# Performance work log

Measured on AMD Instinct MI355X. Metric: run time of the kernel, lower is better.

Reference implementation:

```python
import jax, jax.numpy as jnp
import numpy as np

L, H, E, D, FF, V, CTX = 8, 16, 1024, 64, 4096, 2048, 2048
B, T = 4, 1024


def _ln(x, g, b, eps=1e-5):
    mu = x.mean(-1, keepdims=True)
    var = ((x - mu) ** 2).mean(-1, keepdims=True)
    return (x - mu) * jax.lax.rsqrt(var + eps) * g + b


def setup_inputs() -> dict:
    key = jax.random.key(0)
    ks = jax.random.split(key, 12)
    s = 0.02
    return {
        "tokens": jax.random.randint(ks[0], (B, T), 0, V),
        "tok_emb": jax.random.normal(ks[1], (V, E), jnp.float32) * s,
        "pos_emb": jax.random.normal(ks[2], (CTX, E), jnp.float32) * s,
        "Wq": jax.random.normal(ks[3], (L, H, E, D), jnp.float32) * s,
        "Wk": jax.random.normal(ks[4], (L, H, E, D), jnp.float32) * s,
        "Wv": jax.random.normal(ks[5], (L, H, E, D), jnp.float32) * s,
        "Wo": jax.random.normal(ks[6], (L, H * D, E), jnp.float32) * s,
        "bo": jnp.zeros((L, E), jnp.float32),
        "ln1_g": jnp.ones((L, E), jnp.float32),
        "ln1_b": jnp.zeros((L, E), jnp.float32),
        "ln2_g": jnp.ones((L, E), jnp.float32),
        "ln2_b": jnp.zeros((L, E), jnp.float32),
        "W1": jax.random.normal(ks[7], (L, E, FF), jnp.float32) * s,
        "b1": jnp.zeros((L, FF), jnp.float32),
        "W2": jax.random.normal(ks[8], (L, FF, E), jnp.float32) * s,
        "b2": jnp.zeros((L, E), jnp.float32),
        "lnf_g": jnp.ones((E,), jnp.float32),
        "lnf_b": jnp.zeros((E,), jnp.float32),
        "Wlm": jax.random.normal(ks[9], (E, V), jnp.float32) * s,
        "blm": jnp.zeros((V,), jnp.float32),
    }


def reference(tokens, tok_emb, pos_emb, Wq, Wk, Wv, Wo, bo, ln1_g, ln1_b,
              ln2_g, ln2_b, W1, b1, W2, b2, lnf_g, lnf_b, Wlm, blm):
    # NOTE: original indexes pos_embd with token ids (pos_embd(x.int()))
    x = tok_emb[tokens] + pos_emb[tokens]  # [B,T,E]
    t = x.shape[1]
    causal = jnp.tril(jnp.ones((t, t), bool))
    scale = 1.0 / jnp.sqrt(jnp.float32(D))
    for l in range(L):
        x = _ln(x, ln1_g[l], ln1_b[l])
        q = jnp.einsum('bte,hed->bhtd', x, Wq[l])
        k = jnp.einsum('bte,hed->bhtd', x, Wk[l])
        v = jnp.einsum('bte,hed->bhtd', x, Wv[l])
        scores = jnp.einsum('bhtd,bhsd->bhts', q, k) * scale
        scores = jnp.where(causal, scores, -jnp.inf)
        att = jax.nn.softmax(scores, axis=-1)
        o = jnp.einsum('bhts,bhsd->bhtd', att, v)
        o = o.transpose(0, 2, 1, 3).reshape(x.shape[0], t, H * D)
        x = x + o @ Wo[l] + bo[l]
        x = _ln(x, ln2_g[l], ln2_b[l])
        x = x + jax.nn.relu(x @ W1[l] + b1[l]) @ W2[l] + b2[l]
    x = _ln(x, lnf_g, lnf_b)
    return x @ Wlm + blm
```

## Files before the change

kernel.cpp:

```cpp
#include <hip/hip_runtime.h>
#include <hip/hip_bf16.h>

#define LAYERS 8
#define H_ 16
#define E_ 1024
#define D_ 64
#define FF_ 4096
#define V_ 2048
#define B_ 4
#define T_ 1024
#define MTOK (B_*T_)

typedef __bf16 bf16x8_t __attribute__((ext_vector_type(8)));
typedef __bf16 bf16x4_t __attribute__((ext_vector_type(4)));
typedef float f32x4_t __attribute__((ext_vector_type(4)));
typedef __hip_bfloat16 bf16_t;

__device__ __forceinline__ bf16_t f2b(float f) { return __float2bfloat16(f); }

__global__ void embed_kernel(const int* __restrict__ tokens,
                             const float* __restrict__ te,
                             const float* __restrict__ pe,
                             bf16_t* __restrict__ x) {
  int row = blockIdx.x;
  int tok = tokens[row];
  int t = threadIdx.x;
  float4 va = ((const float4*)(te + (size_t)tok * E_))[t];
  float4 vp = ((const float4*)(pe + (size_t)tok * E_))[t];
  bf16x4_t o;
  o[0] = (__bf16)(va.x + vp.x); o[1] = (__bf16)(va.y + vp.y);
  o[2] = (__bf16)(va.z + vp.z); o[3] = (__bf16)(va.w + vp.w);
  ((bf16x4_t*)(x + (size_t)row * E_))[t] = o;
}

__global__ __launch_bounds__(256) void ln_kernel(const bf16_t* __restrict__ xin,
                                                 bf16_t* __restrict__ xout,
                                                 const float* __restrict__ g,
                                                 const float* __restrict__ b) {
  int tid = threadIdx.x;
  int row = blockIdx.x * 2 + (tid >> 7);
  int li = tid & 127;
  size_t base = (size_t)row * E_ + li * 8;
  bf16x8_t v8 = *(const bf16x8_t*)(xin + base);
  float z[8];
  float s = 0.f, sq = 0.f;
#pragma unroll
  for (int j = 0; j < 8; j++) { z[j] = (float)v8[j]; s += z[j]; sq += z[j] * z[j]; }
  for (int off = 32; off; off >>= 1) {
    s  += __shfl_xor(s, off, 64);
    sq += __shfl_xor(sq, off, 64);
  }
  __shared__ float2 wred[4];
  if ((tid & 63) == 0) wred[tid >> 6] = make_float2(s, sq);
  __syncthreads();
  int wb = (tid >> 7) << 1;
  float S = wred[wb].x + wred[wb + 1].x, SQ = wred[wb].y + wred[wb + 1].y;
  float mean = S * (1.0f / E_);
  float var  = SQ * (1.0f / E_) - mean * mean;
  float inv = rsqrtf(var + 1e-5f);
  float4 g0 = *(const float4*)(g + li * 8), g1 = *(const float4*)(g + li * 8 + 4);
  float4 b0 = *(const float4*)(b + li * 8), b1 = *(const float4*)(b + li * 8 + 4);
  float gg[8] = {g0.x, g0.y, g0.z, g0.w, g1.x, g1.y, g1.z, g1.w};
  float bb[8] = {b0.x, b0.y, b0.z, b0.w, b1.x, b1.y, b1.z, b1.w};
  bf16x8_t o;
#pragma unroll
  for (int j = 0; j < 8; j++) o[j] = (__bf16)((z[j] - mean) * inv * gg[j] + bb[j]);
  *(bf16x8_t*)(xout + base) = o;
}

__global__ __launch_bounds__(256) void reduce_ln_kernel(
    const bf16_t* __restrict__ p,
    const bf16_t* __restrict__ tin,
    const float* __restrict__ bias,
    bf16_t* __restrict__ r,
    bf16_t* __restrict__ tout,
    const float* __restrict__ g,
    const float* __restrict__ b) {
  int tid = threadIdx.x;
  int row = blockIdx.x * 2 + (tid >> 7);
  int li = tid & 127;
  size_t base = (size_t)row * E_ + li * 8;
  bf16x8_t tv = *(const bf16x8_t*)(tin + base);
  bf16x8_t p0 = *(const bf16x8_t*)(p + base);
  bf16x8_t p1 = *(const bf16x8_t*)(p + (size_t)MTOK * E_ + base);
  float4 c0 = *(const float4*)(bias + li * 8), c1 = *(const float4*)(bias + li * 8 + 4);
  float bb[8] = {c0.x, c0.y, c0.z, c0.w, c1.x, c1.y, c1.z, c1.w};
  bf16x8_t rv;
  float z[8];
  float s = 0.f, sq = 0.f;
#pragma unroll
  for (int j = 0; j < 8; j++) {
    float y = (float)tv[j] + (float)p0[j] + (float)p1[j] + bb[j];
    rv[j] = (__bf16)y;
    z[j] = (float)rv[j];
    s += z[j]; sq += z[j] * z[j];
  }
  *(bf16x8_t*)(r + base) = rv;
  for (int off = 32; off; off >>= 1) {
    s  += __shfl_xor(s, off, 64);
    sq += __shfl_xor(sq, off, 64);
  }
  __shared__ float2 wred[4];
  if ((tid & 63) == 0) wred[tid >> 6] = make_float2(s, sq);
  __syncthreads();
  int wb = (tid >> 7) << 1;
  float S = wred[wb].x + wred[wb + 1].x, SQ = wred[wb].y + wred[wb + 1].y;
  float mean = S * (1.0f / E_);
  float var  = SQ * (1.0f / E_) - mean * mean;
  float inv = rsqrtf(var + 1e-5f);
  float4 g0 = *(const float4*)(g + li * 8), g1 = *(const float4*)(g + li * 8 + 4);
  float4 d0 = *(const float4*)(b + li * 8), d1 = *(const float4*)(b + li * 8 + 4);
  float gg[8] = {g0.x, g0.y, g0.z, g0.w, g1.x, g1.y, g1.z, g1.w};
  float dd[8] = {d0.x, d0.y, d0.z, d0.w, d1.x, d1.y, d1.z, d1.w};
  bf16x8_t o;
#pragma unroll
  for (int j = 0; j < 8; j++) o[j] = (__bf16)((z[j] - mean) * inv * gg[j] + dd[j]);
  *(bf16x8_t*)(tout + base) = o;
}

__global__ __launch_bounds__(256) void prep_weights_kernel(
    const float* __restrict__ Wq, const float* __restrict__ Wk,
    const float* __restrict__ Wv, const float* __restrict__ Wo,
    const float* __restrict__ W1, const float* __restrict__ W2,
    bf16_t* __restrict__ WqkvT, bf16_t* __restrict__ WoT,
    bf16_t* __restrict__ W1T, bf16_t* __restrict__ W2T, int l) {
  __shared__ float tile[64][65];
  int bid = blockIdx.x, tid = threadIdx.x;
  const float* src; bf16_t* dst; int R, C, r0, c0;
  if (bid < 768) {
    int op = bid >> 8, rem = bid & 255;
    int h = rem >> 4, tt = rem & 15;
    const float* W = (op == 0) ? Wq : (op == 1) ? Wk : Wv;
    src = W + (size_t)l * H_ * E_ * D_ + (size_t)h * E_ * D_;
    dst = WqkvT + (size_t)op * E_ * H_ * D_ + (size_t)h * E_ * D_;
    R = E_; C = D_; r0 = tt * 64; c0 = 0;
  } else if (bid < 1024) {
    int tt = bid - 768;
    src = Wo + (size_t)l * H_ * D_ * E_; dst = WoT;
    R = H_ * D_; C = E_; r0 = (tt >> 4) * 64; c0 = (tt & 15) * 64;
  } else if (bid < 2048) {
    int tt = bid - 1024;
    src = W1 + (size_t)l * E_ * FF_; dst = W1T;
    R = E_; C = FF_; r0 = (tt >> 6) * 64; c0 = (tt & 63) * 64;
  } else {
    int tt = bid - 2048;
    src = W2 + (size_t)l * FF_ * E_; dst = W2T;
    R = FF_; C = E_; r0 = (tt >> 4) * 64; c0 = (tt & 15) * 64;
  }
#pragma unroll
  for (int i = 0; i < 4; i++) {
    int idx = i * 256 + tid;
    int row = idx >> 4, q4 = (idx & 15) * 4;
    float4 v = *(const float4*)(src + (size_t)(r0 + row) * C + c0 + q4);
    tile[row][q4 + 0] = v.x; tile[row][q4 + 1] = v.y;
    tile[row][q4 + 2] = v.z; tile[row][q4 + 3] = v.w;
  }
  __syncthreads();
#pragma unroll
  for (int i = 0; i < 2; i++) {
    int idx = i * 256 + tid;
    int c = idx >> 3, r8 = (idx & 7) * 8;
    bf16x8_t ov;
#pragma unroll
    for (int j = 0; j < 8; j++) ov[j] = (__bf16)tile[r8 + j][c];
    *(bf16x8_t*)(dst + (size_t)(c0 + c) * R + r0 + r8) = ov;
  }
}

__global__ void transpose_kernel(const float* __restrict__ in, bf16_t* __restrict__ out,
                                 int R, int C) {
  __shared__ float tile[32][33];
  int r0 = blockIdx.y * 32, c0 = blockIdx.x * 32;
  int tx = threadIdx.x, ty = threadIdx.y;
  for (int i = 0; i < 4; i++)
    tile[ty + i * 8][tx] = in[(size_t)(r0 + ty + i * 8) * C + (c0 + tx)];
  __syncthreads();
  for (int i = 0; i < 4; i++)
    out[(size_t)(c0 + ty + i * 8) * R + (r0 + tx)] = f2b(tile[tx][ty + i * 8]);
}

enum { MODE_F32 = 0, MODE_BF16 = 1, MODE_QKV = 2, MODE_BF16R = 3 };

__device__ __forceinline__ void gload16(const bf16_t* g, bf16_t* l) {
  __builtin_amdgcn_global_load_lds((const __attribute__((address_space(1))) void*)g,
                                   (__attribute__((address_space(3))) void*)l, 16, 0, 0);
}

__device__ __forceinline__ int xcd_swz(int flat, int nwg) {
  int q = nwg >> 3, r = nwg & 7;
  int xcd = flat & 7, idx = flat >> 3;
  return (xcd < r ? xcd * (q + 1) : r * (q + 1) + (xcd - r) * q) + idx;
}

#define BK 32
template <int BM, int BN, int MODE>
__global__ __launch_bounds__(256) void gemm97_kernel(
    const bf16_t* __restrict__ A, long long sAz, int lda,
    const bf16_t* __restrict__ Bt, long long sBz, int ldb,
    void* __restrict__ C, long long sCz,
    const float* __restrict__ bias,
    const void* __restrict__ resid,
    int M, int N, int K, int relu) {
  constexpr int FR = BM / 32, FC = BN / 32;
  constexpr int A_ISS = BM / 64, B_ISS = BN / 64;
  __shared__ __align__(16) bf16_t As[2][BM * BK];
  __shared__ __align__(16) bf16_t Bs[2][BN * BK];
  int tid = threadIdx.x;
  int z = blockIdx.z;
  int nwg = gridDim.x * gridDim.y;
  int flat = xcd_swz(blockIdx.y * gridDim.x + blockIdx.x, nwg);
  int m0 = (flat / gridDim.x) * BM, n0 = (flat % gridDim.x) * BN;
  const bf16_t* Ab = A + (size_t)z * sAz + (size_t)m0 * lda;
  const bf16_t* Bb = Bt + (size_t)z * sBz + (size_t)n0 * ldb;
  int lane = tid & 63, wave = tid >> 6;
  int wr = (wave >> 1) * (BM / 2), wc = (wave & 1) * (BN / 2);
  int lr = lane & 15, lk = (lane >> 4) * 8;
  int srow = tid >> 2;
  int scol = (tid & 3) * 8;

  f32x4_t acc[FR][FC];
  for (int i = 0; i < FR; i++)
    for (int j = 0; j < FC; j++)
      acc[i][j] = (f32x4_t){0.f, 0.f, 0.f, 0.f};

  auto stage = [&](int buf, int k0) {
#pragma unroll
    for (int i = 0; i < A_ISS; i++)
      gload16(Ab + (size_t)(i * 64 + srow) * lda + k0 + scol, &As[buf][i * 2048 + wave * 512]);
#pragma unroll
    for (int i = 0; i < B_ISS; i++)
      gload16(Bb + (size_t)(i * 64 + srow) * ldb + k0 + scol, &Bs[buf][i * 2048 + wave * 512]);
  };

  int nk = K / BK;
  stage(0, 0);
  __syncthreads();
  int cur = 0;
  for (int kt = 0; kt < nk; ++kt) {
    if (kt + 1 < nk) stage(cur ^ 1, (kt + 1) * BK);
    bf16x8_t af[FR], bfv[FC];
#pragma unroll
    for (int i = 0; i < FR; i++)
      af[i] = *(const bf16x8_t*)(&As[cur][(wr + i * 16 + lr) * BK + lk]);
#pragma unroll
    for (int j = 0; j < FC; j++)
      bfv[j] = *(const bf16x8_t*)(&Bs[cur][(wc + j * 16 + lr) * BK + lk]);
#pragma unroll
    for (int i = 0; i < FR; i++)
#pragma unroll
      for (int j = 0; j < FC; j++)
        acc[i][j] = __builtin_amdgcn_mfma_f32_16x16x32_bf16(af[i], bfv[j], acc[i][j], 0, 0, 0);
    __syncthreads();
    cur ^= 1;
  }

#pragma unroll
  for (int i = 0; i < FR; i++)
#pragma unroll
    for (int j = 0; j < FC; j++) {
      f32x4_t v = acc[i][j];
      int n = n0 + wc + j * 16 + lr;
      int mb = m0 + wr + i * 16 + (lane >> 4) * 4;
#pragma unroll
      for (int r = 0; r < 4; r++) {
        int m = mb + r;
        float val = v[r];
        if (bias) val += bias[n];
        if (relu) val = fmaxf(val, 0.f);
        if (MODE == MODE_F32) {
          size_t idx = (size_t)z * sCz + (size_t)m * N + n;
          ((float*)C)[idx] = val;
        } else if (MODE == MODE_BF16) {
          size_t idx = (size_t)z * sCz + (size_t)m * N + n;
          ((bf16_t*)C)[idx] = f2b(val);
        } else if (MODE == MODE_BF16R) {
          size_t idx = (size_t)m * N + n;
          val += __bfloat162float(((const bf16_t*)resid)[idx]);
          ((bf16_t*)C)[idx] = f2b(val);
        } else {
          int sect = n >> 10, hd = n & 1023, h = hd >> 6, d = hd & 63;
          int b = m >> 10, t = m & 1023;
          size_t base = (size_t)sect * ((size_t)B_ * H_ * T_ * D_);
          size_t idx = base + ((size_t)(b * H_ + h) << 16) +
                       (sect == 2 ? (size_t)((d << 10) + t) : (size_t)((t << 6) + d));
          ((bf16_t*)C)[idx] = f2b(val);
        }
      }
    }
}

template <int MODE>
__global__ __launch_bounds__(512) void gemm3_kernel(
    const bf16_t* __restrict__ A, int lda,
    const bf16_t* __restrict__ Bt, int ldb,
    void* __restrict__ C, long long sCz,
    const float* __restrict__ bias,
    int M, int N, int kspan, int relu) {
  constexpr int ABUFE = 256 * 64;
  constexpr int BBUFE = 128 * 64;
  __shared__ __align__(16) bf16_t LA[3 * ABUFE];
  __shared__ __align__(16) bf16_t LB[3 * BBUFE];
  int tid = threadIdx.x, lane = tid & 63, wave = tid >> 6;
  int wm = wave >> 1, wn = wave & 1;
  int z = blockIdx.z;
  int nwg = gridDim.x * gridDim.y;
  int flat = xcd_swz(blockIdx.y * gridDim.x + blockIdx.x, nwg);
  int m0 = (flat / gridDim.x) * 256, n0 = (flat % gridDim.x) * 128;
  const bf16_t* Ab = A + (size_t)m0 * lda + (size_t)z * kspan;
  const bf16_t* Bb = Bt + (size_t)n0 * ldb + (size_t)z * kspan;
  int sr = lane & 15, sc = (lane >> 4) * 8;

  f32x4_t acc[4][4];
#pragma unroll
  for (int i = 0; i < 4; i++)
#pragma unroll
    for (int j = 0; j < 4; j++)
      acc[i][j] = (f32x4_t){0.f, 0.f, 0.f, 0.f};

  auto stageh = [&](int b, int kt, int h) {
    int kg = kt * 64;
#pragma unroll
    for (int ch = 0; ch < 2; ch++) {
      int sub = wave * 4 + 2 * h + ch;
      gload16(Ab + (size_t)((sub >> 1) * 16 + sr) * lda + kg + (sub & 1) * 32 + sc,
              LA + b * ABUFE + sub * 512);
    }
    {
      int sub = wave * 2 + h;
      gload16(Bb + (size_t)((sub >> 1) * 16 + sr) * ldb + kg + (sub & 1) * 32 + sc,
              LB + b * BBUFE + sub * 512);
    }
  };

  auto phase = [&](int b, int ks, int t, int nk) {
    bf16x8_t af[4], bfv[4];
    unsigned abase = (unsigned)(size_t)(LA + b * ABUFE);
    unsigned bbase = (unsigned)(size_t)(LB + b * BBUFE);
#pragma unroll
    for (int i = 0; i < 4; i++) {
      unsigned ad = abase + (unsigned)((((wm * 4 + i) * 2 + ks) * 512 + lane * 8) * 2);
      asm volatile("ds_read_b128 %0, %1" : "=v"(af[i]) : "v"(ad));
    }
#pragma unroll
    for (int j = 0; j < 4; j++) {
      unsigned bd = bbase + (unsigned)((((wn * 4 + j) * 2 + ks) * 512 + lane * 8) * 2);
      asm volatile("ds_read_b128 %0, %1" : "=v"(bfv[j]) : "v"(bd));
    }
    if (t + 2 < nk) stageh((t + 2) % 3, t + 2, ks);
    __builtin_amdgcn_s_barrier();
    asm volatile("s_waitcnt lgkmcnt(0)" ::: "memory");
    __builtin_amdgcn_sched_barrier(0);
    __builtin_amdgcn_s_setprio(1);
#pragma unroll
    for (int i = 0; i < 4; i++)
#pragma unroll
      for (int j = 0; j < 4; j++)
        acc[i][j] = __builtin_amdgcn_mfma_f32_16x16x32_bf16(af[i], bfv[j], acc[i][j], 0, 0, 0);
    __builtin_amdgcn_s_setprio(0);
  };

  int nk = kspan / 64;
  stageh(0, 0, 0); stageh(0, 0, 1);
  stageh(1, 1, 0); stageh(1, 1, 1);
  for (int t = 0; t < nk; ++t) {
    int b = t % 3;
    if (t + 1 < nk) { asm volatile("s_waitcnt vmcnt(6)" ::: "memory"); }
    else            { asm volatile("s_waitcnt vmcnt(0)" ::: "memory"); }
    __builtin_amdgcn_s_barrier();
    phase(b, 0, t, nk);
    phase(b, 1, t, nk);
  }

#pragma unroll
  for (int i = 0; i < 4; i++)
#pragma unroll
    for (int j = 0; j < 4; j++) {
      f32x4_t v = acc[i][j];
      int n = n0 + wn * 64 + j * 16 + (lane & 15);
      int mb = m0 + wm * 64 + i * 16 + (lane >> 4) * 4;
#pragma unroll
      for (int r = 0; r < 4; r++) {
        int m = mb + r;
        float val = v[r];
        if (bias) val += bias[n];
        if (relu) val = fmaxf(val, 0.f);
        if (MODE == MODE_F32) {
          size_t idx = (size_t)z * sCz + (size_t)m * N + n;
          ((float*)C)[idx] = val;
        } else {
          size_t idx = (size_t)z * sCz + (size_t)m * N + n;
          ((bf16_t*)C)[idx] = f2b(val);
        }
      }
    }
}

#define KPAD 72

__global__ __launch_bounds__(256) void flash_kernel(
    const bf16_t* __restrict__ q,
    const bf16_t* __restrict__ kk,
    const bf16_t* __restrict__ vt,
    bf16_t* __restrict__ o) {
  __shared__ __align__(16) bf16_t Ks[64 * KPAD];
  __shared__ __align__(16) bf16_t Vs[64 * KPAD];
  __shared__ __align__(16) bf16_t Ps[4][16 * KPAD];
  int bid = blockIdx.x;
  int qi = 15 - (bid >> 6);
  int bh = bid & 63;
  int b = bh >> 4, h = bh & 15;
  const bf16_t* qb = q + ((size_t)bh << 16);
  const bf16_t* kb = kk + ((size_t)bh << 16);
  const bf16_t* vb = vt + ((size_t)bh << 16);
  int tid = threadIdx.x, lane = tid & 63, wave = tid >> 6;
  int lr = lane & 15, lg = lane >> 4;
  int qbase = qi * 64;

  bf16x8_t qf[2];
  {
    const bf16_t* qrow = qb + (size_t)(qbase + wave * 16 + lr) * D_ + lg * 8;
    qf[0] = *(const bf16x8_t*)(qrow);
    qf[1] = *(const bf16x8_t*)(qrow + 32);
  }

  float m_r[4], l_r[4];
  f32x4_t oc[4];
#pragma unroll
  for (int r = 0; r < 4; r++) { m_r[r] = -1e30f; l_r[r] = 0.f; }
#pragma unroll
  for (int j = 0; j < 4; j++) oc[j] = (f32x4_t){0.f, 0.f, 0.f, 0.f};

  int srow = tid >> 2, scol = (tid & 3) * 16;

  bf16x8_t k0, k1, v0, v1;
  {
    const bf16_t* kg = kb + (size_t)srow * D_ + scol;
    k0 = *(const bf16x8_t*)kg;
    k1 = *(const bf16x8_t*)(kg + 8);
    const bf16_t* vg = vb + (size_t)srow * T_ + scol;
    v0 = *(const bf16x8_t*)vg;
    v1 = *(const bf16x8_t*)(vg + 8);
  }

  for (int s = 0; s <= qi; s++) {
    __syncthreads();
    *(bf16x8_t*)(&Ks[srow * KPAD + scol]) = k0;
    *(bf16x8_t*)(&Ks[srow * KPAD + scol + 8]) = k1;
    *(bf16x8_t*)(&Vs[srow * KPAD + scol]) = v0;
    *(bf16x8_t*)(&Vs[srow * KPAD + scol + 8]) = v1;
    __syncthreads();

    if (s < qi) {
      int kv1 = (s + 1) * 64;
      const bf16_t* kg = kb + (size_t)(kv1 + srow) * D_ + scol;
      k0 = *(const bf16x8_t*)kg;
      k1 = *(const bf16x8_t*)(kg + 8);
      const bf16_t* vg = vb + (size_t)srow * T_ + kv1 + scol;
      v0 = *(const bf16x8_t*)vg;
      v1 = *(const bf16x8_t*)(vg + 8);
    }

    int kv0 = s * 64;
    f32x4_t sc[4];
    __builtin_amdgcn_s_setprio(1);
#pragma unroll
    for (int j = 0; j < 4; j++) {
      f32x4_t a = (f32x4_t){0.f, 0.f, 0.f, 0.f};
      bf16x8_t b0 = *(const bf16x8_t*)(&Ks[(j * 16 + lr) * KPAD + lg * 8]);
      bf16x8_t b1 = *(const bf16x8_t*)(&Ks[(j * 16 + lr) * KPAD + lg * 8 + 32]);
      a = __builtin_amdgcn_mfma_f32_16x16x32_bf16(qf[0], b0, a, 0, 0, 0);
      a = __builtin_amdgcn_mfma_f32_16x16x32_bf16(qf[1], b1, a, 0, 0, 0);
      sc[j] = a;
    }
    __builtin_amdgcn_s_setprio(0);
    if (s == qi) {
#pragma unroll
      for (int j = 0; j < 4; j++)
#pragma unroll
        for (int r = 0; r < 4; r++) {
          int kvp = kv0 + j * 16 + lr;
          int qp  = qbase + wave * 16 + lg * 4 + r;
          sc[j][r] = (kvp <= qp) ? sc[j][r] * 0.125f : -1e30f;
        }
    } else {
#pragma unroll
      for (int j = 0; j < 4; j++)
#pragma unroll
        for (int r = 0; r < 4; r++) sc[j][r] *= 0.125f;
    }

    float pm[4];
#pragma unroll
    for (int r = 0; r < 4; r++) {
      float v = fmaxf(fmaxf(sc[0][r], sc[1][r]), fmaxf(sc[2][r], sc[3][r]));
      v = fmaxf(v, __shfl_xor(v, 1, 64));
      v = fmaxf(v, __shfl_xor(v, 2, 64));
      v = fmaxf(v, __shfl_xor(v, 4, 64));
      v = fmaxf(v, __shfl_xor(v, 8, 64));
      pm[r] = v;
    }
    bool ok = (pm[0] - m_r[0] <= 8.f) && (pm[1] - m_r[1] <= 8.f) &&
              (pm[2] - m_r[2] <= 8.f) && (pm[3] - m_r[3] <= 8.f);
    if (!__all(ok)) {
#pragma unroll
      for (int r = 0; r < 4; r++) {
        float mn = fmaxf(m_r[r], pm[r]);
        float ex = __expf(m_r[r] - mn);
        m_r[r] = mn;
        l_r[r] *= ex;
#pragma unroll
        for (int j = 0; j < 4; j++) oc[j][r] *= ex;
      }
    }
#pragma unroll
    for (int j = 0; j < 4; j++)
#pragma unroll
      for (int r = 0; r < 4; r++) {
        float p = __expf(sc[j][r] - m_r[r]);
        l_r[r] += p;
        Ps[wave][(lg * 4 + r) * KPAD + j * 16 + lr] = f2b(p);
      }

    bf16x8_t pa0 = *(const bf16x8_t*)(&Ps[wave][lr * KPAD + lg * 8]);
    bf16x8_t pa1 = *(const bf16x8_t*)(&Ps[wave][lr * KPAD + lg * 8 + 32]);
    __builtin_amdgcn_s_setprio(1);
#pragma unroll
    for (int j = 0; j < 4; j++) {
      bf16x8_t vb0 = *(const bf16x8_t*)(&Vs[(j * 16 + lr) * KPAD + lg * 8]);
      bf16x8_t vb1 = *(const bf16x8_t*)(&Vs[(j * 16 + lr) * KPAD + lg * 8 + 32]);
      oc[j] = __builtin_amdgcn_mfma_f32_16x16x32_bf16(pa0, vb0, oc[j], 0, 0, 0);
      oc[j] = __builtin_amdgcn_mfma_f32_16x16x32_bf16(pa1, vb1, oc[j], 0, 0, 0);
    }
    __builtin_amdgcn_s_setprio(0);
  }

#pragma unroll
  for (int r = 0; r < 4; r++) {
    float v = l_r[r];
    v += __shfl_xor(v, 1, 64);
    v += __shfl_xor(v, 2, 64);
    v += __shfl_xor(v, 4, 64);
    v += __shfl_xor(v, 8, 64);
    l_r[r] = 1.f / v;
  }
  bf16_t* ob = o + ((size_t)(b * T_ + qbase + wave * 16)) * (H_ * D_) + h * D_;
#pragma unroll
  for (int j = 0; j < 4; j++)
#pragma unroll
    for (int r = 0; r < 4; r++) {
      int qrow = lg * 4 + r;
      ob[(size_t)qrow * (H_ * D_) + j * 16 + lr] = f2b(oc[j][r] * l_r[r]);
    }
}

extern "C" void kernel_launch(void* const* d_in, const int* in_sizes, int n_in,
                              void* d_out, int out_size, void* d_ws, size_t ws_size,
                              hipStream_t stream) {
  (void)in_sizes; (void)n_in; (void)out_size; (void)ws_size;
  const int*   tokens = (const int*)d_in[0];
  const float* tok_emb = (const float*)d_in[1];
  const float* pos_emb = (const float*)d_in[2];
  const float* Wq = (const float*)d_in[3];
  const float* Wk = (const float*)d_in[4];
  const float* Wv = (const float*)d_in[5];
  const float* Wo = (const float*)d_in[6];
  const float* bo = (const float*)d_in[7];
  const float* ln1_g = (const float*)d_in[8];
  const float* ln1_b = (const float*)d_in[9];
  const float* ln2_g = (const float*)d_in[10];
  const float* ln2_b = (const float*)d_in[11];
  const float* W1 = (const float*)d_in[12];
  const float* b1 = (const float*)d_in[13];
  const float* W2 = (const float*)d_in[14];
  const float* b2 = (const float*)d_in[15];
  const float* lnf_g = (const float*)d_in[16];
  const float* lnf_b = (const float*)d_in[17];
  const float* Wlm = (const float*)d_in[18];
  const float* blm = (const float*)d_in[19];

  char* w = (char*)d_ws;
  size_t off = 0;
  auto alloc = [&](size_t bytes) { void* p = (void*)(w + off); off += (bytes + 255) & ~(size_t)255; return p; };
  bf16_t* r    = (bf16_t*)alloc((size_t)MTOK * E_ * 2);
  bf16_t* t    = (bf16_t*)alloc((size_t)MTOK * E_ * 2);
  bf16_t* q    = (bf16_t*)alloc((size_t)B_ * H_ * T_ * D_ * 2);
  bf16_t* kk   = (bf16_t*)alloc((size_t)B_ * H_ * T_ * D_ * 2);
  bf16_t* vt   = (bf16_t*)alloc((size_t)B_ * H_ * T_ * D_ * 2);
  bf16_t* o    = (bf16_t*)alloc((size_t)MTOK * E_ * 2);
  bf16_t* h1   = (bf16_t*)alloc((size_t)MTOK * FF_ * 2);
  bf16_t* WqkvT = (bf16_t*)alloc((size_t)3 * E_ * H_ * D_ * 2);
  bf16_t* WoT  = (bf16_t*)alloc((size_t)E_ * H_ * D_ * 2);
  bf16_t* W1T  = (bf16_t*)alloc((size_t)E_ * FF_ * 2);
  bf16_t* W2T  = (bf16_t*)alloc((size_t)E_ * FF_ * 2);
  bf16_t* WlmT = (bf16_t*)alloc((size_t)E_ * V_ * 2);
  bf16_t* p2   = (bf16_t*)alloc((size_t)2 * MTOK * E_ * 2);

  embed_kernel<<<MTOK, 256, 0, stream>>>(tokens, tok_emb, pos_emb, r);
  transpose_kernel<<<dim3(V_ / 32, E_ / 32), dim3(32, 8), 0, stream>>>(Wlm, WlmT, E_, V_);
  ln_kernel<<<MTOK / 2, 256, 0, stream>>>(r, t, ln1_g, ln1_b);

  for (int l = 0; l < LAYERS; l++) {
    prep_weights_kernel<<<3072, 256, 0, stream>>>(
        Wq, Wk, Wv, Wo, W1, W2, WqkvT, WoT, W1T, W2T, l);

    gemm97_kernel<128, 128, MODE_QKV><<<dim3(24, 32, 1), 256, 0, stream>>>(
        t, 0, E_, WqkvT, 0, E_, q, 0, nullptr, nullptr, MTOK, 3 * H_ * D_, E_, 0);

    flash_kernel<<<1024, 256, 0, stream>>>(q, kk, vt, o);

    gemm97_kernel<128, 128, MODE_BF16R><<<dim3(8, 32, 1), 256, 0, stream>>>(
        o, 0, H_ * D_, WoT, 0, H_ * D_, r, 0, bo + l * E_, t, MTOK, E_, H_ * D_, 0);

    ln_kernel<<<MTOK / 2, 256, 0, stream>>>(r, t, ln2_g + l * E_, ln2_b + l * E_);

    gemm3_kernel<MODE_BF16><<<dim3(32, 16, 1), 512, 0, stream>>>(
        t, E_, W1T, E_, h1, 0, b1 + l * FF_, MTOK, FF_, E_, 1);
    gemm3_kernel<MODE_BF16><<<dim3(8, 16, 2), 512, 0, stream>>>(
        h1, FF_, W2T, FF_, p2, (long long)MTOK * E_, nullptr, MTOK, E_, FF_ / 2, 0);
    const float* gn = (l + 1 < LAYERS) ? (ln1_g + (l + 1) * E_) : lnf_g;
    const float* bn = (l + 1 < LAYERS) ? (ln1_b + (l + 1) * E_) : lnf_b;
    reduce_ln_kernel<<<MTOK / 2, 256, 0, stream>>>(p2, t, b2 + l * E_, r, t, gn, bn);
  }

  gemm3_kernel<MODE_F32><<<dim3(16, 16, 1), 512, 0, stream>>>(
      t, E_, WlmT, E_, d_out, 0, blm, MTOK, V_, E_, 0);
}
```

Baseline: 2.076 ms.

## Fuse embedding with first layernorm and transpose V in a separate kernel

The embedding gather is merged with the first layer's layernorm, which removes one kernel launch and one read pass over the residual. The QKV GEMM epilogue now writes V in row-major [t][d] layout, giving coalesced stores in place of the strided transposed scatter. A new per-layer tile transpose kernel then builds the V^T buffer that the flash kernel consumes. This adds an extra launch and an extra read/write of V every layer. The variance is computed as E[x^2]-mean^2, which can differ slightly in numerics.

```diff
diff --git a/kernel.cpp b/kernel.cpp
--- a/kernel.cpp
+++ b/kernel.cpp
@@ -18,19 +18,43 @@
 
 __device__ __forceinline__ bf16_t f2b(float f) { return __float2bfloat16(f); }
 
-__global__ void embed_kernel(const int* __restrict__ tokens,
-                             const float* __restrict__ te,
-                             const float* __restrict__ pe,
-                             bf16_t* __restrict__ x) {
-  int row = blockIdx.x;
+__global__ __launch_bounds__(256) void embed_ln_kernel(const int* __restrict__ tokens,
+                                                       const float* __restrict__ te,
+                                                       const float* __restrict__ pe,
+                                                       bf16_t* __restrict__ r,
+                                                       bf16_t* __restrict__ t,
+                                                       const float* __restrict__ g,
+                                                       const float* __restrict__ b) {
+  int row = blockIdx.x, tid = threadIdx.x;
   int tok = tokens[row];
-  int t = threadIdx.x;
-  float4 va = ((const float4*)(te + (size_t)tok * E_))[t];
-  float4 vp = ((const float4*)(pe + (size_t)tok * E_))[t];
+  float4 va = ((const float4*)(te + (size_t)tok * E_))[tid];
+  float4 vp = ((const float4*)(pe + (size_t)tok * E_))[tid];
+  bf16x4_t rv;
+  rv[0] = (__bf16)(va.x + vp.x); rv[1] = (__bf16)(va.y + vp.y);
+  rv[2] = (__bf16)(va.z + vp.z); rv[3] = (__bf16)(va.w + vp.w);
+  ((bf16x4_t*)(r + (size_t)row * E_))[tid] = rv;
+  float z0 = (float)rv[0], z1 = (float)rv[1], z2 = (float)rv[2], z3 = (float)rv[3];
+  float s = z0 + z1 + z2 + z3, sq = z0*z0 + z1*z1 + z2*z2 + z3*z3;
+  for (int off = 32; off; off >>= 1) {
+    s  += __shfl_xor(s, off, 64);
+    sq += __shfl_xor(sq, off, 64);
+  }
+  __shared__ float2 wred[4];
+  if ((tid & 63) == 0) wred[tid >> 6] = make_float2(s, sq);
+  __syncthreads();
+  float2 w0 = wred[0], w1 = wred[1], w2 = wred[2], w3 = wred[3];
+  float S = w0.x + w1.x + w2.x + w3.x, SQ = w0.y + w1.y + w2.y + w3.y;
+  float mean = S * (1.0f / E_);
+  float var  = SQ * (1.0f / E_) - mean * mean;
+  float inv = rsqrtf(var + 1e-5f);
+  float4 gv = ((const float4*)g)[tid];
+  float4 bv = ((const float4*)b)[tid];
   bf16x4_t o;
-  o[0] = (__bf16)(va.x + vp.x); o[1] = (__bf16)(va.y + vp.y);
-  o[2] = (__bf16)(va.z + vp.z); o[3] = (__bf16)(va.w + vp.w);
-  ((bf16x4_t*)(x + (size_t)row * E_))[t] = o;
+  o[0] = (__bf16)((z0 - mean) * inv * gv.x + bv.x);
+  o[1] = (__bf16)((z1 - mean) * inv * gv.y + bv.y);
+  o[2] = (__bf16)((z2 - mean) * inv * gv.z + bv.z);
+  o[3] = (__bf16)((z3 - mean) * inv * gv.w + bv.w);
+  ((bf16x4_t*)(t + (size_t)row * E_))[tid] = o;
 }
 
 __global__ __launch_bounds__(256) void ln_kernel(const bf16_t* __restrict__ xin,
@@ -179,6 +203,30 @@
     out[(size_t)(c0 + ty + i * 8) * R + (r0 + tx)] = f2b(tile[tx][ty + i * 8]);
 }
 
+__global__ __launch_bounds__(256) void transpose_v_kernel(const bf16_t* __restrict__ v,
+                                                          bf16_t* __restrict__ vt) {
+  __shared__ bf16_t tile[64][72];
+  int bh = blockIdx.y;
+  int t0 = blockIdx.x * 64;
+  const bf16_t* src = v + ((size_t)bh << 16);
+  bf16_t* dst = vt + ((size_t)bh << 16);
+  int tid = threadIdx.x;
+  int row = tid >> 2, c0 = (tid & 3) * 16;
+  bf16x8_t a0 = *(const bf16x8_t*)(src + (size_t)(t0 + row) * D_ + c0);
+  bf16x8_t a1 = *(const bf16x8_t*)(src + (size_t)(t0 + row) * D_ + c0 + 8);
+  *(bf16x8_t*)(&tile[row][c0]) = a0;
+  *(bf16x8_t*)(&tile[row][c0 + 8]) = a1;
+  __syncthreads();
+  int drow = tid >> 2, tc0 = (tid & 3) * 16;
+  bf16x8_t o0, o1;
+#pragma unroll
+  for (int j = 0; j < 8; j++) o0[j] = tile[tc0 + j][drow];
+#pragma unroll
+  for (int j = 0; j < 8; j++) o1[j] = tile[tc0 + 8 + j][drow];
+  *(bf16x8_t*)(dst + (size_t)drow * T_ + t0 + tc0) = o0;
+  *(bf16x8_t*)(dst + (size_t)drow * T_ + t0 + tc0 + 8) = o1;
+}
+
 enum { MODE_F32 = 0, MODE_BF16 = 1, MODE_QKV = 2, MODE_BF16R = 3 };
 
 __device__ __forceinline__ void gload16(const bf16_t* g, bf16_t* l) {
@@ -281,8 +329,7 @@
           int sect = n >> 10, hd = n & 1023, h = hd >> 6, d = hd & 63;
           int b = m >> 10, t = m & 1023;
           size_t base = (size_t)sect * ((size_t)B_ * H_ * T_ * D_);
-          size_t idx = base + ((size_t)(b * H_ + h) << 16) +
-                       (sect == 2 ? (size_t)((d << 10) + t) : (size_t)((t << 6) + d));
+          size_t idx = base + ((size_t)(b * H_ + h) << 16) + (t << 6) + d;
           ((bf16_t*)C)[idx] = f2b(val);
         }
       }
@@ -585,6 +632,7 @@
   bf16_t* t    = (bf16_t*)alloc((size_t)MTOK * E_ * 2);
   bf16_t* q    = (bf16_t*)alloc((size_t)B_ * H_ * T_ * D_ * 2);
   bf16_t* kk   = (bf16_t*)alloc((size_t)B_ * H_ * T_ * D_ * 2);
+  bf16_t* v    = (bf16_t*)alloc((size_t)B_ * H_ * T_ * D_ * 2);
   bf16_t* vt   = (bf16_t*)alloc((size_t)B_ * H_ * T_ * D_ * 2);
   bf16_t* o    = (bf16_t*)alloc((size_t)MTOK * E_ * 2);
   bf16_t* h1   = (bf16_t*)alloc((size_t)MTOK * FF_ * 2);
@@ -595,9 +643,8 @@
   bf16_t* WlmT = (bf16_t*)alloc((size_t)E_ * V_ * 2);
   bf16_t* p2   = (bf16_t*)alloc((size_t)2 * MTOK * E_ * 2);
 
-  embed_kernel<<<MTOK, 256, 0, stream>>>(tokens, tok_emb, pos_emb, r);
+  embed_ln_kernel<<<MTOK, 256, 0, stream>>>(tokens, tok_emb, pos_emb, r, t, ln1_g, ln1_b);
   transpose_kernel<<<dim3(V_ / 32, E_ / 32), dim3(32, 8), 0, stream>>>(Wlm, WlmT, E_, V_);
-  ln_kernel<<<MTOK / 2, 256, 0, stream>>>(r, t, ln1_g, ln1_b);
 
   for (int l = 0; l < LAYERS; l++) {
     prep_weights_kernel<<<3072, 256, 0, stream>>>(
@@ -605,6 +652,8 @@
 
     gemm97_kernel<128, 128, MODE_QKV><<<dim3(24, 32, 1), 256, 0, stream>>>(
         t, 0, E_, WqkvT, 0, E_, q, 0, nullptr, nullptr, MTOK, 3 * H_ * D_, E_, 0);
+
+    transpose_v_kernel<<<dim3(T_ / 64, B_ * H_), 256, 0, stream>>>(v, vt);
 
     flash_kernel<<<1024, 256, 0, stream>>>(q, kk, vt, o);
 
```

Result: no change. 2.063 ms (-0.6%).
